# Optimization experiments

Measured on AMD Instinct MI355X. Metric: run time of the kernel, lower is better.

## Reference

```python
import jax, jax.numpy as jnp
import numpy as np

B = 4096      # batch size per view (init arg bs)
D = 256       # embedding dim
TEMP = 0.5    # init arg temp
EPS = 1e-8    # torch CosineSimilarity eps


def setup_inputs() -> dict:
    key = jax.random.key(0)
    k1, k2 = jax.random.split(key)
    return {
        "emb1": jax.random.normal(k1, (B, D), dtype=jnp.float32),
        "emb2": jax.random.normal(k2, (B, D), dtype=jnp.float32),
    }


def reference(emb1, emb2):
    # z: (2B, D)
    z = jnp.concatenate([emb1, emb2], axis=0)
    n = 2 * B
    # Cosine similarity as normalize + GEMM (same math as broadcast CosineSimilarity):
    # sim[i,j] = (z_i . z_j) / max(||z_i||*||z_j||, eps), then / temp
    norms = jnp.linalg.norm(z, axis=-1)                       # (2B,)
    denom = jnp.maximum(norms[:, None] * norms[None, :], EPS)  # (2B,2B)
    sim = (z @ z.T) / denom / TEMP                             # (2B,2B)

    idx = jnp.arange(n)
    # positives: diag(sim, +B) then diag(sim, -B) == sim[i, (i+B) mod 2B]
    pos = sim[idx, (idx + B) % n]                              # (2B,)

    # logits row i = [pos_i, negatives_i] = all sim[i,:] except the diagonal.
    # cross-entropy with label 0: loss_i = -pos_i + logsumexp(row without diag)
    diag_mask = idx[:, None] == idx[None, :]
    sim_masked = jnp.where(diag_mask, -jnp.inf, sim)
    lse = jax.nn.logsumexp(sim_masked, axis=-1)                # (2B,)

    loss = jnp.sum(lse - pos) / n   # CrossEntropyLoss(reduction='sum') / 2B
    return loss
```

## Files before the change

kernel.cpp:

```cpp
#include <hip/hip_runtime.h>
#include <hip/hip_bf16.h>


constexpr int kN  = 8192;
constexpr int kD  = 256;
constexpr int kBH = 4096;
constexpr int kChunks  = 32;
constexpr int kColsPer = kN / kChunks;
constexpr int kNT = kColsPer / 16;
constexpr float kSqrtScale = 1.6986436f;
constexpr float kLn2 = 0.6931471805599453f;

typedef __attribute__((ext_vector_type(8))) short bf16x8;
typedef __attribute__((ext_vector_type(4))) float f32x4;

__device__ __forceinline__ unsigned short f2bf(float f) {
  union { float f; unsigned u; } x;
  x.f = f;
  unsigned u = x.u;
  return (unsigned short)((u + 0x7FFFu + ((u >> 16) & 1u)) >> 16);
}
__device__ __forceinline__ float bf2f(unsigned short h) {
  union { unsigned u; float f; } x;
  x.u = ((unsigned)h) << 16;
  return x.f;
}
__device__ __forceinline__ void gload_lds16(const short* g, short* l) {
  __builtin_amdgcn_global_load_lds(
      (const __attribute__((address_space(1))) void*)g,
      (__attribute__((address_space(3))) void*)l, 16, 0, 0);
}

__global__ void k_normalize(const float* __restrict__ e1,
                            const float* __restrict__ e2,
                            unsigned short* __restrict__ zn,
                            float* __restrict__ s_sum) {
  if (blockIdx.x < 8) {
    float4 z4 = {0.f, 0.f, 0.f, 0.f};
    *reinterpret_cast<float4*>(s_sum + blockIdx.x * 1024 + threadIdx.x * 4) = z4;
  }
  const int wave = threadIdx.x >> 6;
  const int lane = threadIdx.x & 63;
  const int row  = blockIdx.x * 4 + wave;
  const float* src = (row < kBH) ? (e1 + (size_t)row * kD)
                                 : (e2 + (size_t)(row - kBH) * kD);
  float4 v = *reinterpret_cast<const float4*>(src + lane * 4);
  float ssq = v.x * v.x + v.y * v.y + v.z * v.z + v.w * v.w;
#pragma unroll
  for (int m = 1; m < 64; m <<= 1) ssq += __shfl_xor(ssq, m);
  const float invs = kSqrtScale / sqrtf(ssq);
  ushort4 o;
  o.x = f2bf(v.x * invs);
  o.y = f2bf(v.y * invs);
  o.z = f2bf(v.z * invs);
  o.w = f2bf(v.w * invs);
  const int g  = row >> 4;
  const int rr = row & 15;
  const size_t dst = (size_t)g * 4096 + (lane >> 3) * 512 +
                     ((lane >> 1) & 3) * 128 + rr * 8 + (lane & 1) * 4;
  *reinterpret_cast<ushort4*>(zn + dst) = o;
}

__global__ void k_pos(const unsigned short* __restrict__ zn,
                      float* __restrict__ pos_val,
                      float* __restrict__ dacc) {
  const int wave = threadIdx.x >> 6;
  const int lane = threadIdx.x & 63;
  const int i = blockIdx.x * 4 + wave;
  const int j = i + kBH;
  const int rr = i & 15;
  const size_t off = (size_t)(i >> 4) * 4096 + (lane >> 3) * 512 +
                     ((lane >> 1) & 3) * 128 + rr * 8 + (lane & 1) * 4;
  ushort4 ua = *reinterpret_cast<const ushort4*>(zn + off);
  ushort4 ub = *reinterpret_cast<const ushort4*>(zn + off + (size_t)256 * 4096);
  float dij = 0.f, dii = 0.f, djj = 0.f;
  const unsigned short* pa = &ua.x;
  const unsigned short* pb = &ub.x;
#pragma unroll
  for (int q = 0; q < 4; ++q) {
    const float a = bf2f(pa[q]);
    const float b = bf2f(pb[q]);
    dij += a * b;
    dii += a * a;
    djj += b * b;
  }
#pragma unroll
  for (int m = 1; m < 64; m <<= 1) {
    dij += __shfl_xor(dij, m);
    dii += __shfl_xor(dii, m);
    djj += __shfl_xor(djj, m);
  }
  if (lane == 0) {
    const float p = dij * kLn2;
    pos_val[i] = p;
    pos_val[j] = p;
    dacc[i] = dii;
    dacc[j] = djj;
  }
}

__global__ __launch_bounds__(256, 4)
void k_simlse(const unsigned short* __restrict__ zn,
              float* __restrict__ s_sum) {
  __shared__ __align__(16) short ldsB[4][4096];

  const int bid = blockIdx.x;
  const int rt  = bid >> 5;
  const int ch  = bid & 31;
  const int wave = threadIdx.x >> 6;
  const int lane = threadIdx.x & 63;
  const int l15 = lane & 15;
  const int lhi = lane >> 4;
  const int rowBase = rt * 128 + wave * 32;
  const int grpBase = ch * kNT;

  bf16x8 a0[8], a1[8];
  {
    const unsigned short* ap = zn + (size_t)(rowBase >> 4) * 4096 + lane * 8;
#pragma unroll
    for (int ks = 0; ks < 8; ++ks) {
      a0[ks] = *reinterpret_cast<const bf16x8*>(ap + ks * 512);
      a1[ks] = *reinterpret_cast<const bf16x8*>(ap + 4096 + ks * 512);
    }
  }

  auto stage = [&](int t) {
    const short* src = (const short*)zn +
                       (size_t)(grpBase + (t & (kNT - 1))) * 4096 + wave * 1024;
    short* dst = &ldsB[t & 3][wave * 1024];
    gload_lds16(src + lane * 8, dst);
    gload_lds16(src + 512 + lane * 8, dst + 512);
  };

  stage(0);
  stage(1);
  stage(2);
  asm volatile("s_waitcnt vmcnt(0)" ::: "memory");

  float sacc[2][4] = {{0.f,0.f,0.f,0.f},{0.f,0.f,0.f,0.f}};

#pragma unroll 1
  for (int t = 0; t < kNT; ++t) {
    asm volatile("s_waitcnt vmcnt(4)" ::: "memory");
    __builtin_amdgcn_s_barrier();
    stage(t + 3);

    const short* bt = &ldsB[t & 3][0];
    bf16x8 b[8];
#pragma unroll
    for (int ks = 0; ks < 8; ++ks)
      b[ks] = *reinterpret_cast<const bf16x8*>(bt + ks * 512 + lane * 8);

    f32x4 acc0 = {0.f,0.f,0.f,0.f};
    f32x4 acc1 = {0.f,0.f,0.f,0.f};
    __builtin_amdgcn_s_setprio(1);
#pragma unroll
    for (int ks = 0; ks < 8; ++ks) {
      acc0 = __builtin_amdgcn_mfma_f32_16x16x32_bf16(a0[ks], b[ks], acc0, 0, 0, 0);
      acc1 = __builtin_amdgcn_mfma_f32_16x16x32_bf16(a1[ks], b[ks], acc1, 0, 0, 0);
    }
    __builtin_amdgcn_s_setprio(0);
#pragma unroll
    for (int j = 0; j < 4; ++j) {
      sacc[0][j] += exp2f(acc0[j]);
      sacc[1][j] += exp2f(acc1[j]);
    }
  }

#pragma unroll
  for (int s = 0; s < 2; ++s) {
#pragma unroll
    for (int j = 0; j < 4; ++j) {
      float sv = sacc[s][j];
#pragma unroll
      for (int m = 1; m < 16; m <<= 1) sv += __shfl_xor(sv, m);
      if (l15 == 0) {
        const int row = rowBase + s * 16 + lhi * 4 + j;
        atomicAdd(&s_sum[row], sv);
      }
    }
  }
}

__global__ void k_final(const float* __restrict__ s_sum,
                        const float* __restrict__ dacc,
                        const float* __restrict__ pos_val,
                        float* __restrict__ out) {
  __shared__ float red[16];
  float acc = 0.0f;
  for (int r = threadIdx.x; r < kN; r += 1024)
    acc += logf(s_sum[r] - exp2f(dacc[r])) - pos_val[r];
#pragma unroll
  for (int m = 1; m < 64; m <<= 1) acc += __shfl_xor(acc, m);
  const int wave = threadIdx.x >> 6;
  const int lane = threadIdx.x & 63;
  if (lane == 0) red[wave] = acc;
  __syncthreads();
  if (threadIdx.x == 0) {
    float t = 0.0f;
#pragma unroll
    for (int w = 0; w < 16; ++w) t += red[w];
    out[0] = t / (float)kN;
  }
}

extern "C" void kernel_launch(void* const* d_in, const int* in_sizes, int n_in,
                              void* d_out, int out_size, void* d_ws, size_t ws_size,
                              hipStream_t stream) {
  const float* e1 = (const float*)d_in[0];
  const float* e2 = (const float*)d_in[1];
  float* out = (float*)d_out;

  unsigned short* zn = (unsigned short*)d_ws;
  float* s_sum   = (float*)((char*)d_ws + (size_t)kN * kD * 2);
  float* dacc    = s_sum + kN;
  float* pos_val = dacc + kN;

  hipLaunchKernelGGL(k_normalize, dim3(kN / 4), dim3(256), 0, stream,
                     e1, e2, zn, s_sum);
  hipLaunchKernelGGL(k_pos, dim3(kBH / 4), dim3(256), 0, stream,
                     zn, pos_val, dacc);
  hipLaunchKernelGGL(k_simlse, dim3(64 * kChunks), dim3(256), 0, stream,
                     zn, s_sum);
  hipLaunchKernelGGL(k_final, dim3(1), dim3(1024), 0, stream,
                     s_sum, dacc, pos_val, out);
}
```

Before: 57.73 us.

## Exploit similarity matrix symmetry to compute only upper-triangle tiles

Before, each block computed a 128x256 slab, so the whole 8192x8192 similarity matrix was evaluated. Now each block computes a 128x128 tile, and only tiles on or above the diagonal are scheduled (row tile plus an offset 0..31, plus the 32 tiles at offset 32). Off-diagonal tiles add their exp sums into both the row sums and, through an LDS column reduction, the column sums. This roughly halves MFMA and exp work, at the cost of extra shuffles, LDS writes, a block barrier and more atomics per tile.

```diff
diff --git a/kernel.cpp b/kernel.cpp
--- a/kernel.cpp
+++ b/kernel.cpp
@@ -5,9 +5,9 @@
 constexpr int kN  = 8192;
 constexpr int kD  = 256;
 constexpr int kBH = 4096;
-constexpr int kChunks  = 32;
-constexpr int kColsPer = kN / kChunks;
-constexpr int kNT = kColsPer / 16;
+constexpr int kTile = 128;
+constexpr int kNT = kTile / 16;
+constexpr int kGrid = 64 * 32 + 32;
 constexpr float kSqrtScale = 1.6986436f;
 constexpr float kLn2 = 0.6931471805599453f;
 
@@ -103,16 +103,24 @@
 void k_simlse(const unsigned short* __restrict__ zn,
               float* __restrict__ s_sum) {
   __shared__ __align__(16) short ldsB[4][4096];
+  __shared__ float ldsCol[4][kTile];
 
   const int bid = blockIdx.x;
-  const int rt  = bid >> 5;
-  const int ch  = bid & 31;
+  int rt, ct;
+  if (bid < 2048) {
+    rt = bid >> 5;
+    ct = (rt + (bid & 31)) & 63;
+  } else {
+    rt = bid - 2048;
+    ct = rt + 32;
+  }
+  const bool offDiag = (rt != ct);
   const int wave = threadIdx.x >> 6;
   const int lane = threadIdx.x & 63;
   const int l15 = lane & 15;
   const int lhi = lane >> 4;
-  const int rowBase = rt * 128 + wave * 32;
-  const int grpBase = ch * kNT;
+  const int rowBase = rt * kTile + wave * 32;
+  const int grpBase = ct * kNT;
 
   bf16x8 a0[8], a1[8];
   {
@@ -160,11 +168,20 @@
       acc1 = __builtin_amdgcn_mfma_f32_16x16x32_bf16(a1[ks], b[ks], acc1, 0, 0, 0);
     }
     __builtin_amdgcn_s_setprio(0);
+
+    float p0[4], p1[4];
 #pragma unroll
     for (int j = 0; j < 4; ++j) {
-      sacc[0][j] += exp2f(acc0[j]);
-      sacc[1][j] += exp2f(acc1[j]);
-    }
+      p0[j] = exp2f(acc0[j]);
+      p1[j] = exp2f(acc1[j]);
+      sacc[0][j] += p0[j];
+      sacc[1][j] += p1[j];
+    }
+    float cs = ((p0[0] + p0[1]) + (p0[2] + p0[3])) +
+               ((p1[0] + p1[1]) + (p1[2] + p1[3]));
+    cs += __shfl_xor(cs, 16);
+    cs += __shfl_xor(cs, 32);
+    if (lhi == 0) ldsCol[wave][t * 16 + l15] = cs;
   }
 
 #pragma unroll
@@ -178,6 +195,15 @@
         const int row = rowBase + s * 16 + lhi * 4 + j;
         atomicAdd(&s_sum[row], sv);
       }
+    }
+  }
+
+  if (offDiag) {
+    __syncthreads();
+    for (int c = threadIdx.x; c < kTile; c += 256) {
+      const float v = (ldsCol[0][c] + ldsCol[1][c]) +
+                      (ldsCol[2][c] + ldsCol[3][c]);
+      atomicAdd(&s_sum[ct * kTile + c], v);
     }
   }
 }
@@ -220,7 +246,7 @@
                      e1, e2, zn, s_sum);
   hipLaunchKernelGGL(k_pos, dim3(kBH / 4), dim3(256), 0, stream,
                      zn, pos_val, dacc);
-  hipLaunchKernelGGL(k_simlse, dim3(64 * kChunks), dim3(256), 0, stream,
+  hipLaunchKernelGGL(k_simlse, dim3(kGrid), dim3(256), 0, stream,
                      zn, s_sum);
   hipLaunchKernelGGL(k_final, dim3(1), dim3(1024), 0, stream,
                      s_sum, dacc, pos_val, out);
```

Result: faster. 53.15 us (median of 2 runs) (-7.9%).

## Exploit similarity-matrix symmetry with triangular 256x256 tiles and row+column sums

Applied to the files above, without the earlier changes.

Replaces the row-tile-by-column-chunk grid with a triangular grid of 256x256 tiles covering only the upper triangle. Each off-diagonal tile's exp2 values feed both the row sums and, through a column reduction, the column sums. Both operands are staged through triple-buffered LDS, with 8 waves per block each computing a 128x64 sub-tile. This roughly halves MFMA and exp work, at the cost of more atomics, a larger accumulator register footprint, and load imbalance on diagonal tiles.

```diff
diff --git a/kernel.cpp b/kernel.cpp
--- a/kernel.cpp
+++ b/kernel.cpp
@@ -5,9 +5,10 @@
 constexpr int kN  = 8192;
 constexpr int kD  = 256;
 constexpr int kBH = 4096;
-constexpr int kChunks  = 32;
-constexpr int kColsPer = kN / kChunks;
-constexpr int kNT = kColsPer / 16;
+constexpr int kST = 256;
+constexpr int kNRT = kN / kST;
+constexpr int kGrid = kNRT * (kNRT + 1) / 2;
+constexpr int kKS = kD / 32;
 constexpr float kSqrtScale = 1.6986436f;
 constexpr float kLn2 = 0.6931471805599453f;
 
@@ -99,84 +100,112 @@
   }
 }
 
-__global__ __launch_bounds__(256, 4)
+__global__ __launch_bounds__(512, 2)
 void k_simlse(const unsigned short* __restrict__ zn,
               float* __restrict__ s_sum) {
-  __shared__ __align__(16) short ldsB[4][4096];
+  __shared__ __align__(16) short ldsA[3][8192];
+  __shared__ __align__(16) short ldsB[3][8192];
 
   const int bid = blockIdx.x;
-  const int rt  = bid >> 5;
-  const int ch  = bid & 31;
-  const int wave = threadIdx.x >> 6;
-  const int lane = threadIdx.x & 63;
+  int rt = (int)((sqrtf(8.0f * bid + 1.0f) - 1.0f) * 0.5f);
+  while ((rt + 1) * (rt + 2) / 2 <= bid) ++rt;
+  while (rt * (rt + 1) / 2 > bid) --rt;
+  const int ct = bid - rt * (rt + 1) / 2;
+  const bool offDiag = (rt != ct);
+
+  const int tid = threadIdx.x;
+  const int wave = tid >> 6;
+  const int wr = wave >> 2;
+  const int wc = wave & 3;
+  const int lane = tid & 63;
   const int l15 = lane & 15;
   const int lhi = lane >> 4;
-  const int rowBase = rt * 128 + wave * 32;
-  const int grpBase = ch * kNT;
-
-  bf16x8 a0[8], a1[8];
-  {
-    const unsigned short* ap = zn + (size_t)(rowBase >> 4) * 4096 + lane * 8;
-#pragma unroll
-    for (int ks = 0; ks < 8; ++ks) {
-      a0[ks] = *reinterpret_cast<const bf16x8*>(ap + ks * 512);
-      a1[ks] = *reinterpret_cast<const bf16x8*>(ap + 4096 + ks * 512);
-    }
-  }
-
-  auto stage = [&](int t) {
-    const short* src = (const short*)zn +
-                       (size_t)(grpBase + (t & (kNT - 1))) * 4096 + wave * 1024;
-    short* dst = &ldsB[t & 3][wave * 1024];
-    gload_lds16(src + lane * 8, dst);
-    gload_lds16(src + 512 + lane * 8, dst + 512);
+  const int rowSup = rt * kST;
+  const int colSup = ct * kST;
+  const int gA = (rowSup >> 4);
+  const int gB = (colSup >> 4);
+
+  auto stage = [&](int kk) {
+    const int ks = kk & 7;
+    const int buf = kk % 3;
+    const short* zs = (const short*)zn;
+    gload_lds16(zs + (size_t)(gA + wave) * 4096 + ks * 512 + lane * 8,
+                &ldsA[buf][wave * 512 + lane * 8]);
+    gload_lds16(zs + (size_t)(gA + 8 + wave) * 4096 + ks * 512 + lane * 8,
+                &ldsA[buf][(8 + wave) * 512 + lane * 8]);
+    gload_lds16(zs + (size_t)(gB + wave) * 4096 + ks * 512 + lane * 8,
+                &ldsB[buf][wave * 512 + lane * 8]);
+    gload_lds16(zs + (size_t)(gB + 8 + wave) * 4096 + ks * 512 + lane * 8,
+                &ldsB[buf][(8 + wave) * 512 + lane * 8]);
   };
+
+  f32x4 acc[8][4];
+#pragma unroll
+  for (int g = 0; g < 8; ++g)
+#pragma unroll
+    for (int c = 0; c < 4; ++c) acc[g][c] = {0.f, 0.f, 0.f, 0.f};
 
   stage(0);
   stage(1);
-  stage(2);
   asm volatile("s_waitcnt vmcnt(0)" ::: "memory");
 
-  float sacc[2][4] = {{0.f,0.f,0.f,0.f},{0.f,0.f,0.f,0.f}};
-
 #pragma unroll 1
-  for (int t = 0; t < kNT; ++t) {
+  for (int kk = 0; kk < kKS; ++kk) {
     asm volatile("s_waitcnt vmcnt(4)" ::: "memory");
     __builtin_amdgcn_s_barrier();
-    stage(t + 3);
-
-    const short* bt = &ldsB[t & 3][0];
-    bf16x8 b[8];
-#pragma unroll
-    for (int ks = 0; ks < 8; ++ks)
-      b[ks] = *reinterpret_cast<const bf16x8*>(bt + ks * 512 + lane * 8);
-
-    f32x4 acc0 = {0.f,0.f,0.f,0.f};
-    f32x4 acc1 = {0.f,0.f,0.f,0.f};
+    stage(kk + 2);
+
+    const short* pA = &ldsA[kk % 3][0];
+    const short* pB = &ldsB[kk % 3][0];
+    bf16x8 bfr[4];
+#pragma unroll
+    for (int c = 0; c < 4; ++c)
+      bfr[c] = *reinterpret_cast<const bf16x8*>(pB + (wc * 4 + c) * 512 + lane * 8);
     __builtin_amdgcn_s_setprio(1);
 #pragma unroll
-    for (int ks = 0; ks < 8; ++ks) {
-      acc0 = __builtin_amdgcn_mfma_f32_16x16x32_bf16(a0[ks], b[ks], acc0, 0, 0, 0);
-      acc1 = __builtin_amdgcn_mfma_f32_16x16x32_bf16(a1[ks], b[ks], acc1, 0, 0, 0);
+    for (int g = 0; g < 8; ++g) {
+      const bf16x8 afr =
+          *reinterpret_cast<const bf16x8*>(pA + (wr * 8 + g) * 512 + lane * 8);
+#pragma unroll
+      for (int c = 0; c < 4; ++c)
+        acc[g][c] = __builtin_amdgcn_mfma_f32_16x16x32_bf16(afr, bfr[c], acc[g][c], 0, 0, 0);
     }
     __builtin_amdgcn_s_setprio(0);
+  }
+
+  float csum[4] = {0.f, 0.f, 0.f, 0.f};
+#pragma unroll
+  for (int g = 0; g < 8; ++g) {
+    float rs[4] = {0.f, 0.f, 0.f, 0.f};
+#pragma unroll
+    for (int c = 0; c < 4; ++c) {
+      float p0 = exp2f(acc[g][c][0]);
+      float p1 = exp2f(acc[g][c][1]);
+      float p2 = exp2f(acc[g][c][2]);
+      float p3 = exp2f(acc[g][c][3]);
+      rs[0] += p0; rs[1] += p1; rs[2] += p2; rs[3] += p3;
+      csum[c] += (p0 + p1) + (p2 + p3);
+    }
 #pragma unroll
     for (int j = 0; j < 4; ++j) {
-      sacc[0][j] += exp2f(acc0[j]);
-      sacc[1][j] += exp2f(acc1[j]);
-    }
-  }
-
-#pragma unroll
-  for (int s = 0; s < 2; ++s) {
-#pragma unroll
-    for (int j = 0; j < 4; ++j) {
-      float sv = sacc[s][j];
+      float sv = rs[j];
 #pragma unroll
       for (int m = 1; m < 16; m <<= 1) sv += __shfl_xor(sv, m);
       if (l15 == 0) {
-        const int row = rowBase + s * 16 + lhi * 4 + j;
+        const int row = rowSup + wr * 128 + g * 16 + lhi * 4 + j;
         atomicAdd(&s_sum[row], sv);
+      }
+    }
+  }
+  if (offDiag) {
+#pragma unroll
+    for (int c = 0; c < 4; ++c) {
+      float cv = csum[c];
+      cv += __shfl_xor(cv, 16);
+      cv += __shfl_xor(cv, 32);
+      if (lhi == 0) {
+        const int col = colSup + wc * 64 + c * 16 + l15;
+        atomicAdd(&s_sum[col], cv);
       }
     }
   }
@@ -220,7 +249,7 @@
                      e1, e2, zn, s_sum);
   hipLaunchKernelGGL(k_pos, dim3(kBH / 4), dim3(256), 0, stream,
                      zn, pos_val, dacc);
-  hipLaunchKernelGGL(k_simlse, dim3(64 * kChunks), dim3(256), 0, stream,
+  hipLaunchKernelGGL(k_simlse, dim3(kGrid), dim3(512), 0, stream,
                      zn, s_sum);
   hipLaunchKernelGGL(k_final, dim3(1), dim3(1024), 0, stream,
                      s_sum, dacc, pos_val, out);
```

After: 79.84 us. 1.38x slower.
